# Kernel optimization log

Measured on AMD Instinct MI355X. Metric: run time of the kernel, lower is better.

## Reference

```python
import jax, jax.numpy as jnp
import numpy as np


def setup_inputs() -> dict:
    mesh = 2048
    N = mesh * mesh
    key = jax.random.key(0)
    k1, k2, k3, k4, k5 = jax.random.split(key, 5)
    theta = jax.random.normal(k1, (N - 1,), dtype=jnp.float32) * 1e-4
    phi = jax.random.normal(k2, (N - 1,), dtype=jnp.float32) * 1e-4
    psi = jax.random.normal(k3, (N - 1,), dtype=jnp.float32) * 1e-4
    state_re = jax.random.normal(k4, (N, 2, 1), dtype=jnp.float32)
    state_im = jax.random.normal(k5, (N, 2, 1), dtype=jnp.float32)
    # normalize spinors so |<s|s>| = 1 (physical states are normalized)
    norm = jnp.sqrt(jnp.sum(state_re**2 + state_im**2, axis=(1, 2), keepdims=True))
    state_re = state_re / norm
    state_im = state_im / norm
    return {"theta": theta, "phi": phi, "psi": psi,
            "state_re": state_re, "state_im": state_im}


def _deform(theta, phi, psi, state_re, state_im):
    # per-site SU(2) matrices, [N-1, 2, 2]
    ct, st = jnp.cos(theta), jnp.sin(theta)
    cp, sp = jnp.cos(phi), jnp.sin(phi)
    cq, sq = jnp.cos(psi), jnp.sin(psi)
    su_re = jnp.stack([jnp.stack([ct * cp, -st * cq], -1),
                       jnp.stack([st * cq, ct * cp], -1)], -2)  # [N-1,2,2]
    su_im = jnp.stack([jnp.stack([ct * sp, -st * sq], -1),
                       jnp.stack([-st * sq, -ct * sp], -1)], -2)
    d_re = jnp.einsum('nij,njk->nik', su_re, state_re[1:]) - \
           jnp.einsum('nij,njk->nik', su_im, state_im[1:])
    d_im = jnp.einsum('nij,njk->nik', su_re, state_im[1:]) + \
           jnp.einsum('nij,njk->nik', su_im, state_re[1:])
    def_re = jnp.concatenate([state_re[:1], d_re], axis=0)
    def_im = jnp.concatenate([state_im[:1], d_im], axis=0)
    return def_re, def_im


def _hs_distance(a_re, a_im, b_re, b_im):
    # Hilbert-Schmidt distance between 2-spinors, elementwise over leading dims
    rr = jnp.sum(a_re * b_re + a_im * b_im, axis=-1)
    ri = jnp.sum(a_re * b_im - a_im * b_re, axis=-1)
    return jnp.sqrt(jnp.abs(1.0 - rr**2 - ri**2))


def reference(theta, phi, psi, state_re, state_im):
    N = state_re.shape[0]
    mesh = int(np.sqrt(N))
    def_re, def_im = _deform(theta, phi, psi, state_re, state_im)
    # [mesh, mesh, 2] grids
    g_re = def_re.reshape(mesh, mesh, 2)
    g_im = def_im.reshape(mesh, mesh, 2)
    # v: neighbor at (i, j+1) with wrap; h: (i+1, j); d: (i+1, j+1)
    v = _hs_distance(g_re, g_im,
                     jnp.roll(g_re, -1, axis=1), jnp.roll(g_im, -1, axis=1))
    h = _hs_distance(g_re, g_im,
                     jnp.roll(g_re, -1, axis=0), jnp.roll(g_im, -1, axis=0))
    d = _hs_distance(g_re, g_im,
                     jnp.roll(jnp.roll(g_re, -1, axis=0), -1, axis=1),
                     jnp.roll(jnp.roll(g_im, -1, axis=0), -1, axis=1))
    return jnp.stack([v, h, d])  # [3, mesh, mesh]
```

## Files before the change

### kernel.cpp

```cpp
#include <hip/hip_runtime.h>
#include <math.h>

#define TILE_I 8
#define TILE_J 32
#define HALO_I (TILE_I + 1)
#define HALO_J (TILE_J + 1)

__global__ __launch_bounds__(256) void qwz_deform_dirichlet_kernel(
    const float* __restrict__ theta,
    const float* __restrict__ phi,
    const float* __restrict__ psi,
    const float2* __restrict__ sre,
    const float2* __restrict__ sim,
    float* __restrict__ out,
    int mesh)
{
    const int N = mesh * mesh;
    __shared__ float4 tile[HALO_I * HALO_J];

    const int bi = blockIdx.y * TILE_I;
    const int bj = blockIdx.x * TILE_J;
    const int tid = threadIdx.x;

    for (int l = tid; l < HALO_I * HALO_J; l += 256) {
        int ti = l / HALO_J;
        int tj = l - ti * HALO_J;
        int gi = bi + ti; if (gi >= mesh) gi -= mesh;
        int gj = bj + tj; if (gj >= mesh) gj -= mesh;
        int n = gi * mesh + gj;

        float2 r = sre[n];
        float2 im = sim[n];
        float4 d4;
        if (n == 0) {
            d4 = make_float4(r.x, r.y, im.x, im.y);
        } else {
            float th = theta[n - 1], ph = phi[n - 1], ps = psi[n - 1];
            float st, ct, sp, cp, sq, cq;
            __sincosf(th, &st, &ct);
            __sincosf(ph, &sp, &cp);
            __sincosf(ps, &sq, &cq);
            float a = ct * cp;
            float b = st * cq;
            float c = ct * sp;
            float d = st * sq;
            d4.x = a * r.x - b * r.y - c * im.x + d * im.y;
            d4.y = b * r.x + a * r.y + d * im.x + c * im.y;
            d4.z = a * im.x - b * im.y + c * r.x - d * r.y;
            d4.w = b * im.x + a * im.y - d * r.x - c * r.y;
        }
        tile[l] = d4;
    }
    __syncthreads();

    int ti = tid >> 5;
    int tj = tid & 31;
    float4 A = tile[ti * HALO_J + tj];
    float4 V = tile[ti * HALO_J + tj + 1];
    float4 H = tile[(ti + 1) * HALO_J + tj];
    float4 D = tile[(ti + 1) * HALO_J + tj + 1];

    int gi = bi + ti;
    int gj = bj + tj;
    int site = gi * mesh + gj;

    {
        float rr = A.x * V.x + A.y * V.y + A.z * V.z + A.w * V.w;
        float ri = A.x * V.z + A.y * V.w - A.z * V.x - A.w * V.y;
        out[site] = sqrtf(fabsf(1.0f - rr * rr - ri * ri));
    }
    {
        float rr = A.x * H.x + A.y * H.y + A.z * H.z + A.w * H.w;
        float ri = A.x * H.z + A.y * H.w - A.z * H.x - A.w * H.y;
        out[N + site] = sqrtf(fabsf(1.0f - rr * rr - ri * ri));
    }
    {
        float rr = A.x * D.x + A.y * D.y + A.z * D.z + A.w * D.w;
        float ri = A.x * D.z + A.y * D.w - A.z * D.x - A.w * D.y;
        out[2 * N + site] = sqrtf(fabsf(1.0f - rr * rr - ri * ri));
    }
}

extern "C" void kernel_launch(void* const* d_in, const int* in_sizes, int n_in,
                              void* d_out, int out_size, void* d_ws, size_t ws_size,
                              hipStream_t stream) {
    const float* theta = (const float*)d_in[0];
    const float* phi   = (const float*)d_in[1];
    const float* psi   = (const float*)d_in[2];
    const float2* sre  = (const float2*)d_in[3];
    const float2* sim  = (const float2*)d_in[4];
    float* out = (float*)d_out;

    int N = in_sizes[0] + 1;
    int mesh = (int)(sqrt((double)N) + 0.5);

    dim3 grid(mesh / TILE_J, mesh / TILE_I);
    dim3 block(256);
    qwz_deform_dirichlet_kernel<<<grid, block, 0, stream>>>(
        theta, phi, psi, sre, sim, out, mesh);
}
```

Baseline: 165.8 us.

## Enlarge stencil tile to 32x32 with per-thread column reuse and batched loads

Switches from 8x32 to 32x32 output tiles so halo recomputation of the deformed spinors shrinks. Each thread now computes four vertically adjacent outputs and reuses shared-memory column values between rows. All global loads for the halo fill are issued up front before any sincos work to expose memory parallelism, and outputs use nontemporal stores. This costs more registers and shared memory per block and gives fewer blocks in the grid.

```diff
diff --git a/kernel.cpp b/kernel.cpp
--- a/kernel.cpp
+++ b/kernel.cpp
@@ -1,10 +1,9 @@
 #include <hip/hip_runtime.h>
 #include <math.h>
 
-#define TILE_I 8
-#define TILE_J 32
-#define HALO_I (TILE_I + 1)
-#define HALO_J (TILE_J + 1)
+#define TILE 32
+#define HALO 33
+#define NHALO (HALO * HALO)
 
 __global__ __launch_bounds__(256) void qwz_deform_dirichlet_kernel(
     const float* __restrict__ theta,
@@ -16,68 +15,88 @@
     int mesh)
 {
     const int N = mesh * mesh;
-    __shared__ float4 tile[HALO_I * HALO_J];
+    __shared__ float4 tile[NHALO];
 
-    const int bi = blockIdx.y * TILE_I;
-    const int bj = blockIdx.x * TILE_J;
+    const int bi = blockIdx.y * TILE;
+    const int bj = blockIdx.x * TILE;
     const int tid = threadIdx.x;
 
-    for (int l = tid; l < HALO_I * HALO_J; l += 256) {
-        int ti = l / HALO_J;
-        int tj = l - ti * HALO_J;
-        int gi = bi + ti; if (gi >= mesh) gi -= mesh;
-        int gj = bj + tj; if (gj >= mesh) gj -= mesh;
+    float th[5], ph[5], ps[5];
+    float2 r2[5], i2[5];
+    int n_arr[5];
+#pragma unroll
+    for (int k = 0; k < 5; ++k) {
+        int l = tid + k * 256;
+        int trow = l / HALO;
+        int tcol = l - trow * HALO;
+        int gi = bi + trow; if (gi >= mesh) gi -= mesh;
+        int gj = bj + tcol; if (gj >= mesh) gj -= mesh;
         int n = gi * mesh + gj;
+        n_arr[k] = n;
+        int an = (n > 0) ? n - 1 : 0;
+        th[k] = theta[an];
+        ph[k] = phi[an];
+        ps[k] = psi[an];
+        r2[k] = sre[n];
+        i2[k] = sim[n];
+    }
 
-        float2 r = sre[n];
-        float2 im = sim[n];
+#pragma unroll
+    for (int k = 0; k < 5; ++k) {
+        int l = tid + k * 256;
+        float st, ct, sp, cp, sq, cq;
+        __sincosf(th[k], &st, &ct);
+        __sincosf(ph[k], &sp, &cp);
+        __sincosf(ps[k], &sq, &cq);
+        float a = ct * cp;
+        float b = st * cq;
+        float c = ct * sp;
+        float d = st * sq;
+        float2 r = r2[k], im = i2[k];
         float4 d4;
-        if (n == 0) {
+        d4.x = a * r.x - b * r.y - c * im.x + d * im.y;
+        d4.y = b * r.x + a * r.y + d * im.x + c * im.y;
+        d4.z = a * im.x - b * im.y + c * r.x - d * r.y;
+        d4.w = b * im.x + a * im.y - d * r.x - c * r.y;
+        if (n_arr[k] == 0)
             d4 = make_float4(r.x, r.y, im.x, im.y);
-        } else {
-            float th = theta[n - 1], ph = phi[n - 1], ps = psi[n - 1];
-            float st, ct, sp, cp, sq, cq;
-            __sincosf(th, &st, &ct);
-            __sincosf(ph, &sp, &cp);
-            __sincosf(ps, &sq, &cq);
-            float a = ct * cp;
-            float b = st * cq;
-            float c = ct * sp;
-            float d = st * sq;
-            d4.x = a * r.x - b * r.y - c * im.x + d * im.y;
-            d4.y = b * r.x + a * r.y + d * im.x + c * im.y;
-            d4.z = a * im.x - b * im.y + c * r.x - d * r.y;
-            d4.w = b * im.x + a * im.y - d * r.x - c * r.y;
-        }
-        tile[l] = d4;
+        if (l < NHALO)
+            tile[l] = d4;
     }
     __syncthreads();
 
-    int ti = tid >> 5;
-    int tj = tid & 31;
-    float4 A = tile[ti * HALO_J + tj];
-    float4 V = tile[ti * HALO_J + tj + 1];
-    float4 H = tile[(ti + 1) * HALO_J + tj];
-    float4 D = tile[(ti + 1) * HALO_J + tj + 1];
+    const int trow = (tid >> 5) << 2;
+    const int tcol = tid & 31;
 
-    int gi = bi + ti;
-    int gj = bj + tj;
-    int site = gi * mesh + gj;
+    float4 c0[5], c1[5];
+#pragma unroll
+    for (int k = 0; k < 5; ++k) {
+        c0[k] = tile[(trow + k) * HALO + tcol];
+        c1[k] = tile[(trow + k) * HALO + tcol + 1];
+    }
 
-    {
-        float rr = A.x * V.x + A.y * V.y + A.z * V.z + A.w * V.w;
-        float ri = A.x * V.z + A.y * V.w - A.z * V.x - A.w * V.y;
-        out[site] = sqrtf(fabsf(1.0f - rr * rr - ri * ri));
-    }
-    {
-        float rr = A.x * H.x + A.y * H.y + A.z * H.z + A.w * H.w;
-        float ri = A.x * H.z + A.y * H.w - A.z * H.x - A.w * H.y;
-        out[N + site] = sqrtf(fabsf(1.0f - rr * rr - ri * ri));
-    }
-    {
-        float rr = A.x * D.x + A.y * D.y + A.z * D.z + A.w * D.w;
-        float ri = A.x * D.z + A.y * D.w - A.z * D.x - A.w * D.y;
-        out[2 * N + site] = sqrtf(fabsf(1.0f - rr * rr - ri * ri));
+#pragma unroll
+    for (int k = 0; k < 4; ++k) {
+        float4 A = c0[k];
+        float4 V = c1[k];
+        float4 H = c0[k + 1];
+        float4 D = c1[k + 1];
+        int site = (bi + trow + k) * mesh + (bj + tcol);
+
+        float rr, ri, v, h, d;
+        rr = A.x * V.x + A.y * V.y + A.z * V.z + A.w * V.w;
+        ri = A.x * V.z + A.y * V.w - A.z * V.x - A.w * V.y;
+        v = sqrtf(fabsf(1.0f - rr * rr - ri * ri));
+        rr = A.x * H.x + A.y * H.y + A.z * H.z + A.w * H.w;
+        ri = A.x * H.z + A.y * H.w - A.z * H.x - A.w * H.y;
+        h = sqrtf(fabsf(1.0f - rr * rr - ri * ri));
+        rr = A.x * D.x + A.y * D.y + A.z * D.z + A.w * D.w;
+        ri = A.x * D.z + A.y * D.w - A.z * D.x - A.w * D.y;
+        d = sqrtf(fabsf(1.0f - rr * rr - ri * ri));
+
+        __builtin_nontemporal_store(v, out + site);
+        __builtin_nontemporal_store(h, out + N + site);
+        __builtin_nontemporal_store(d, out + 2 * N + site);
     }
 }
 
@@ -94,7 +113,7 @@
     int N = in_sizes[0] + 1;
     int mesh = (int)(sqrt((double)N) + 0.5);
 
-    dim3 grid(mesh / TILE_J, mesh / TILE_I);
+    dim3 grid(mesh / TILE, mesh / TILE);
     dim3 block(256);
     qwz_deform_dirichlet_kernel<<<grid, block, 0, stream>>>(
         theta, phi, psi, sre, sim, out, mesh);
```

Result: no change. 163.9 us (-1.1%).

## Stream rows per wavefront with shuffles instead of shared-memory halo tiles

Applied to the files above, without the earlier changes.

Replaces the 2D shared-memory halo tile with a per-wave column-band scheme: each wave covers 63 columns, marches down 16 rows keeping the current and next deformed row in registers, and gets the right neighbour via wave shuffles. This cuts the halo recomputation overhead (sincos and loads for halo cells) from ~(9*33)/(8*32) to ~(17*64)/(16*63), removes the LDS sync, and software-prefetches the next row. It also uses nontemporal stores for the outputs. It relies on mesh being a power of two for the mask-based wraparound.

```diff
diff --git a/kernel.cpp b/kernel.cpp
--- a/kernel.cpp
+++ b/kernel.cpp
@@ -1,10 +1,64 @@
 #include <hip/hip_runtime.h>
 #include <math.h>
 
-#define TILE_I 8
-#define TILE_J 32
-#define HALO_I (TILE_I + 1)
-#define HALO_J (TILE_J + 1)
+#define ROWS  16
+#define BANDW 63
+#define WAVES_PER_BLOCK 4
+
+struct Raw {
+    float th, ph, ps;
+    float2 r, im;
+    int n;
+};
+
+__device__ inline Raw load_row(const float* __restrict__ theta,
+                               const float* __restrict__ phi,
+                               const float* __restrict__ psi,
+                               const float2* __restrict__ sre,
+                               const float2* __restrict__ sim,
+                               int i, int j, int mesh, int mask) {
+    Raw w;
+    int n = (i & mask) * mesh + j;
+    w.n = n;
+    int an = (n > 0) ? n - 1 : 0;
+    w.th = theta[an];
+    w.ph = phi[an];
+    w.ps = psi[an];
+    w.r  = sre[n];
+    w.im = sim[n];
+    return w;
+}
+
+__device__ inline float4 deform(const Raw& w) {
+    float st, ct, sp, cp, sq, cq;
+    __sincosf(w.th, &st, &ct);
+    __sincosf(w.ph, &sp, &cp);
+    __sincosf(w.ps, &sq, &cq);
+    float a = ct * cp, b = st * cq, c = ct * sp, d = st * sq;
+    float4 o;
+    o.x = a * w.r.x - b * w.r.y - c * w.im.x + d * w.im.y;
+    o.y = b * w.r.x + a * w.r.y + d * w.im.x + c * w.im.y;
+    o.z = a * w.im.x - b * w.im.y + c * w.r.x - d * w.r.y;
+    o.w = b * w.im.x + a * w.im.y - d * w.r.x - c * w.r.y;
+    if (w.n == 0)
+        o = make_float4(w.r.x, w.r.y, w.im.x, w.im.y);
+    return o;
+}
+
+__device__ inline float4 shfl_down4(float4 v) {
+    float4 o;
+    o.x = __shfl_down(v.x, 1, 64);
+    o.y = __shfl_down(v.y, 1, 64);
+    o.z = __shfl_down(v.z, 1, 64);
+    o.w = __shfl_down(v.w, 1, 64);
+    return o;
+}
+
+__device__ inline float hs_dist(const float4& A, const float4& B) {
+    float rr = A.x * B.x + A.y * B.y + A.z * B.z + A.w * B.w;
+    float ri = A.x * B.z + A.y * B.w - A.z * B.x - A.w * B.y;
+    return sqrtf(fabsf(1.0f - rr * rr - ri * ri));
+}
 
 __global__ __launch_bounds__(256) void qwz_deform_dirichlet_kernel(
     const float* __restrict__ theta,
@@ -16,68 +70,38 @@
     int mesh)
 {
     const int N = mesh * mesh;
-    __shared__ float4 tile[HALO_I * HALO_J];
+    const int mask = mesh - 1;
+    const int lane = threadIdx.x & 63;
+    const int wave = threadIdx.x >> 6;
+    const int band = blockIdx.x * WAVES_PER_BLOCK + wave;
+    const int j_raw = band * BANDW + lane;
+    const int j = j_raw & mask;
+    const int i0 = blockIdx.y * ROWS;
+    const bool emit = (lane < BANDW) && (j_raw < mesh);
 
-    const int bi = blockIdx.y * TILE_I;
-    const int bj = blockIdx.x * TILE_J;
-    const int tid = threadIdx.x;
+    Raw a = load_row(theta, phi, psi, sre, sim, i0, j, mesh, mask);
+    Raw b = load_row(theta, phi, psi, sre, sim, i0 + 1, j, mesh, mask);
+    float4 cur = deform(a);
 
-    for (int l = tid; l < HALO_I * HALO_J; l += 256) {
-        int ti = l / HALO_J;
-        int tj = l - ti * HALO_J;
-        int gi = bi + ti; if (gi >= mesh) gi -= mesh;
-        int gj = bj + tj; if (gj >= mesh) gj -= mesh;
-        int n = gi * mesh + gj;
+    for (int k = 0; k < ROWS; ++k) {
+        Raw c = load_row(theta, phi, psi, sre, sim, i0 + k + 2, j, mesh, mask);
+        float4 nxt = deform(b);
 
-        float2 r = sre[n];
-        float2 im = sim[n];
-        float4 d4;
-        if (n == 0) {
-            d4 = make_float4(r.x, r.y, im.x, im.y);
-        } else {
-            float th = theta[n - 1], ph = phi[n - 1], ps = psi[n - 1];
-            float st, ct, sp, cp, sq, cq;
-            __sincosf(th, &st, &ct);
-            __sincosf(ph, &sp, &cp);
-            __sincosf(ps, &sq, &cq);
-            float a = ct * cp;
-            float b = st * cq;
-            float c = ct * sp;
-            float d = st * sq;
-            d4.x = a * r.x - b * r.y - c * im.x + d * im.y;
-            d4.y = b * r.x + a * r.y + d * im.x + c * im.y;
-            d4.z = a * im.x - b * im.y + c * r.x - d * r.y;
-            d4.w = b * im.x + a * im.y - d * r.x - c * r.y;
+        float4 V = shfl_down4(cur);
+        float4 D = shfl_down4(nxt);
+
+        float v = hs_dist(cur, V);
+        float h = hs_dist(cur, nxt);
+        float d = hs_dist(cur, D);
+
+        if (emit) {
+            int site = (i0 + k) * mesh + j_raw;
+            __builtin_nontemporal_store(v, out + site);
+            __builtin_nontemporal_store(h, out + N + site);
+            __builtin_nontemporal_store(d, out + 2 * N + site);
         }
-        tile[l] = d4;
-    }
-    __syncthreads();
-
-    int ti = tid >> 5;
-    int tj = tid & 31;
-    float4 A = tile[ti * HALO_J + tj];
-    float4 V = tile[ti * HALO_J + tj + 1];
-    float4 H = tile[(ti + 1) * HALO_J + tj];
-    float4 D = tile[(ti + 1) * HALO_J + tj + 1];
-
-    int gi = bi + ti;
-    int gj = bj + tj;
-    int site = gi * mesh + gj;
-
-    {
-        float rr = A.x * V.x + A.y * V.y + A.z * V.z + A.w * V.w;
-        float ri = A.x * V.z + A.y * V.w - A.z * V.x - A.w * V.y;
-        out[site] = sqrtf(fabsf(1.0f - rr * rr - ri * ri));
-    }
-    {
-        float rr = A.x * H.x + A.y * H.y + A.z * H.z + A.w * H.w;
-        float ri = A.x * H.z + A.y * H.w - A.z * H.x - A.w * H.y;
-        out[N + site] = sqrtf(fabsf(1.0f - rr * rr - ri * ri));
-    }
-    {
-        float rr = A.x * D.x + A.y * D.y + A.z * D.z + A.w * D.w;
-        float ri = A.x * D.z + A.y * D.w - A.z * D.x - A.w * D.y;
-        out[2 * N + site] = sqrtf(fabsf(1.0f - rr * rr - ri * ri));
+        cur = nxt;
+        b = c;
     }
 }
 
@@ -94,8 +118,10 @@
     int N = in_sizes[0] + 1;
     int mesh = (int)(sqrt((double)N) + 0.5);
 
-    dim3 grid(mesh / TILE_J, mesh / TILE_I);
-    dim3 block(256);
+    int bands = (mesh + BANDW - 1) / BANDW;
+    int gx = (bands + WAVES_PER_BLOCK - 1) / WAVES_PER_BLOCK;
+    dim3 grid(gx, mesh / ROWS);
+    dim3 block(64 * WAVES_PER_BLOCK);
     qwz_deform_dirichlet_kernel<<<grid, block, 0, stream>>>(
         theta, phi, psi, sre, sim, out, mesh);
 }
```

Result: slower. 174.3 us (+5.2%).
